# Performance work log

Hardware: AMD Instinct MI355X
Metric: run time of the kernel (lower is better)

Reference implementation:

```python
import jax, jax.numpy as jnp
import numpy as np

J, L = 4, 8
M = N = 128
B = 2
EPS = 1e-6  # abs_eps smoothing: |z|_eps = sqrt(re^2 + im^2 + eps)


def indices_third_order(J, L):
    # For each bandpass filter i = j1*L + l1, pair with every filter of scale
    # j2 >= j1 (all L angles) plus the lowpass (index J*L).
    # Count = J*L*(L*(J+1)/2 + 1) == num_coefficients.
    i_list, j_list = [], []
    for j1 in range(J):
        for l1 in range(L):
            i = j1 * L + l1
            for j2 in range(j1, J):
                for l2 in range(L):
                    i_list.append(i)
                    j_list.append(j2 * L + l2)
            i_list.append(i)
            j_list.append(J * L)
    return np.asarray(i_list), np.asarray(j_list)


def make_filters(J, L, M, N):
    # Real frequency-domain Morlet-like Gaussian bumps at J scales x L angles,
    # plus one lowpass. Shape (1, J*L+1, M, N), float32.
    kx = 2.0 * np.pi * np.fft.fftfreq(M)[:, None]
    ky = 2.0 * np.pi * np.fft.fftfreq(N)[None, :]
    filts = []
    for j in range(J):
        k0 = 0.8 * np.pi / 2.0 ** j
        sigma = 0.5 * k0
        for l in range(L):
            theta = np.pi * l / L
            cx, cy = k0 * np.cos(theta), k0 * np.sin(theta)
            filts.append(np.exp(-((kx - cx) ** 2 + (ky - cy) ** 2) / (2.0 * sigma ** 2)))
    sigma_lp = 0.8 * np.pi / 2.0 ** J
    filts.append(np.exp(-(kx ** 2 + ky ** 2) / (2.0 * sigma_lp ** 2)))
    return np.stack(filts)[None].astype(np.float32)


def abs_eps(z):
    return jnp.sqrt(z.real ** 2 + z.imag ** 2 + EPS)


def setup_inputs() -> dict:
    key = jax.random.key(0)
    x = jax.random.normal(key, (B, 1, M, N), dtype=jnp.float32)
    filters = jnp.asarray(make_filters(J, L, M, N))  # (1, 33, M, N)
    return {"x": x, "filters": filters}


def reference(x, filters):
    idx0, idx1 = indices_third_order(J, L)
    # first-order filtering: (B, nf, M, N) complex
    xf = jnp.fft.ifft2(filters * jnp.fft.fft2(x))
    xa = abs_eps(xf)  # real (B, nf, M, N)
    # cross-scale correlation: (B, nf_i, nf_j, M, N)
    inner = jnp.fft.ifft2(filters[:, None] * jnp.fft.fft2(xa)[:, :, None])
    out = jnp.real(jnp.conj(xf)[:, None] * inner).mean(axis=(-2, -1))  # (B, nf, nf)
    return out[:, idx0, idx1]  # (B, 672)
```

## Files before the change

kernel.cpp:

```cpp
#include <hip/hip_runtime.h>
#include <math.h>


#define PI_F 3.14159265358979323846f

__device__ __forceinline__ void make_tw(int lane, float* twr, float* twi) {
#pragma unroll
  for (int s = 0; s < 6; ++s) {
    int h = 32 >> s;
    float ang = -PI_F * (float)(lane & (h - 1)) / (float)h;
    float sv, cv;
    sincosf(ang, &sv, &cv);
    twr[s] = cv; twi[s] = sv;
  }
  float ang = -PI_F * (float)lane / 64.0f;
  float sv, cv;
  sincosf(ang, &sv, &cv);
  twr[6] = cv; twi[6] = sv;
}

template <int S>
__device__ __forceinline__ void fft128_dif(float& ar, float& ai, float& br, float& bi,
                                           const float* twr, const float* twi, int lane) {
  float s6r = twr[6], s6i = (S > 0) ? twi[6] : -twi[6];
  float ur = ar + br, ui = ai + bi;
  float vr = ar - br, vi = ai - bi;
  ar = ur; ai = ui;
  br = vr * s6r - vi * s6i;
  bi = vr * s6i + vi * s6r;
#pragma unroll
  for (int s = 0; s < 6; ++s) {
    int h = 32 >> s;
    float wr = twr[s], wi = (S > 0) ? twi[s] : -twi[s];
    bool hi = (lane & h) != 0;
    float pr, pi2;
    pr = __shfl_xor(ar, h, 64); pi2 = __shfl_xor(ai, h, 64);
    if (!hi) { ar += pr; ai += pi2; }
    else { float dr = pr - ar, di = pi2 - ai; ar = dr * wr - di * wi; ai = dr * wi + di * wr; }
    pr = __shfl_xor(br, h, 64); pi2 = __shfl_xor(bi, h, 64);
    if (!hi) { br += pr; bi += pi2; }
    else { float dr = pr - br, di = pi2 - bi; br = dr * wr - di * wi; bi = dr * wi + di * wr; }
  }
}

__device__ __forceinline__ void transpose_r2c(float (&dr)[16], float (&di)[16],
    float (&er)[8], float (&ei)[8], float (&fr)[8], float (&fi2)[8],
    float2 (*tile)[128], int lane, int w) {
#pragma unroll
  for (int ch = 0; ch < 2; ++ch) {
    if ((w >> 3) == ch) {
#pragma unroll
      for (int t = 0; t < 8; ++t) {
        int r = w * 8 + t;
        int rr = r & 63, sw = r & 15;
        tile[rr][lane ^ sw] = make_float2(dr[2 * t], di[2 * t]);
        tile[rr][(lane + 64) ^ sw] = make_float2(dr[2 * t + 1], di[2 * t + 1]);
      }
    }
    __syncthreads();
    {
      int sw = lane & 15;
#pragma unroll
      for (int ci = 0; ci < 8; ++ci) {
        int c = w * 8 + ci;
        float2 v = tile[lane][c ^ sw];
        if (ch == 0) { er[ci] = v.x; ei[ci] = v.y; }
        else { fr[ci] = v.x; fi2[ci] = v.y; }
      }
    }
    __syncthreads();
  }
}

__global__ __launch_bounds__(1024, 2) void k_prep(const float* __restrict__ x,
    float2* __restrict__ X, float* __restrict__ out) {
  __shared__ float2 tile[64][128];
  int tid = threadIdx.x;
  if (blockIdx.x == 2) {
    if (tid < 1344) out[tid] = 0.f;
    if (tid < 320) out[tid + 1024] = 0.f;
    return;
  }
  int b = blockIdx.x;
  int lane = tid & 63, w = tid >> 6;
  float twr[7], twi[7]; make_tw(lane, twr, twi);
  const float* xb = x + b * 16384;
  float dr[16], di[16];
  float er[8], ei[8], fr[8], fi2[8];
#pragma unroll
  for (int t = 0; t < 8; ++t) {
    int r = w * 8 + t;
    float ar = xb[r * 128 + lane], ai2 = 0.f, br = xb[r * 128 + lane + 64], bi = 0.f;
    fft128_dif<1>(ar, ai2, br, bi, twr, twi, lane);
    dr[2 * t] = ar; di[2 * t] = ai2; dr[2 * t + 1] = br; di[2 * t + 1] = bi;
  }
  transpose_r2c(dr, di, er, ei, fr, fi2, tile, lane, w);
  int u0 = __brev((unsigned)lane) >> 25;
#pragma unroll
  for (int ci = 0; ci < 8; ++ci) {
    int c = w * 8 + ci;
    float ar = er[ci], ai2 = ei[ci], br = fr[ci], bi = fi2[ci];
    fft128_dif<1>(ar, ai2, br, bi, twr, twi, lane);
    int vn = __brev((unsigned)c) >> 25;
    X[b * 16384 + u0 * 128 + vn] = make_float2(ar, ai2);
    X[b * 16384 + (u0 + 1) * 128 + vn] = make_float2(br, bi);
  }
}

__global__ __launch_bounds__(1024, 2) void k_fields(const float2* __restrict__ X,
    const float* __restrict__ F, float* __restrict__ dfld, float* __restrict__ xa) {
  __shared__ float2 tile[64][128];
  int tid = threadIdx.x, lane = tid & 63, w = tid >> 6;
  bool isd = (blockIdx.x < 66);
  int b, f;
  float* optr;
  if (isd) {
    b = blockIdx.x / 33; f = blockIdx.x - b * 33;
    optr = dfld + blockIdx.x * 16384;
  } else {
    int q = blockIdx.x - 66; b = q >> 5; f = q & 31;
    optr = xa + q * 16384;
  }
  const float* Fb = F + f * 16384;
  float twr[7], twi[7]; make_tw(lane, twr, twi);
  const float2* Xb = X + b * 16384;
  float dr[16], di[16];
  float er[8], ei[8], fr[8], fi2[8];

#pragma unroll
  for (int t = 0; t < 8; ++t) {
    int r = w * 8 + t;
    float2 x0 = Xb[r * 128 + lane];
    float2 x1 = Xb[r * 128 + lane + 64];
    float f0 = Fb[r * 128 + lane], f1 = Fb[r * 128 + lane + 64];
    if (isd) { f0 *= f0; f1 *= f1; }
    float ar = x0.x * f0, ai2 = x0.y * f0, br = x1.x * f1, bi = x1.y * f1;
    fft128_dif<-1>(ar, ai2, br, bi, twr, twi, lane);
    dr[2 * t] = ar; di[2 * t] = ai2; dr[2 * t + 1] = br; di[2 * t + 1] = bi;
  }
  transpose_r2c(dr, di, er, ei, fr, fi2, tile, lane, w);

  const float sc = 1.0f / 16384.0f;
#pragma unroll
  for (int ci = 0; ci < 8; ++ci) {
    int c = w * 8 + ci;
    float ar = er[ci], ai2 = ei[ci], br = fr[ci], bi = fi2[ci];
    fft128_dif<-1>(ar, ai2, br, bi, twr, twi, lane);
    if (isd) {
      optr[c * 128 + lane] = ar;
      optr[c * 128 + lane + 64] = br;
    } else {
      float t0r = ar * sc, t0i = ai2 * sc, t1r = br * sc, t1i = bi * sc;
      optr[c * 128 + lane] = sqrtf(t0r * t0r + t0i * t0i + 1e-6f);
      optr[c * 128 + lane + 64] = sqrtf(t1r * t1r + t1i * t1i + 1e-6f);
    }
  }
}

__global__ __launch_bounds__(512) void k_dot(const float* __restrict__ xa,
    const float* __restrict__ dfld, float* __restrict__ out) {
  int im = blockIdx.x >> 2;
  int slice = blockIdx.x & 3;
  int b = im >> 5, i = im & 31;
  int t = threadIdx.x;
  const float* xr = xa + im * 16384 + slice * 4096;
  const float* db = dfld + b * 33 * 16384 + slice * 4096;
  float acc[33];
#pragma unroll
  for (int j = 0; j < 33; ++j) acc[j] = 0.f;
#pragma unroll
  for (int it = 0; it < 8; ++it) {
    int k = it * 512 + t;
    float xv = xr[k];
#pragma unroll
    for (int j = 0; j < 33; ++j) acc[j] += xv * db[j * 16384 + k];
  }
#pragma unroll
  for (int j = 0; j < 33; ++j) {
#pragma unroll
    for (int off = 32; off > 0; off >>= 1) acc[j] += __shfl_xor(acc[j], off, 64);
  }
  __shared__ float red[8][33];
  int w = t >> 6, lane = t & 63;
  if (lane == 0) {
#pragma unroll
    for (int j = 0; j < 33; ++j) red[w][j] = acc[j];
  }
  __syncthreads();
  if (t < 33) {
    float s = 0.f;
#pragma unroll
    for (int w2 = 0; w2 < 8; ++w2) s += red[w2][t];
    int j = t;
    int j1 = i >> 3, l1 = i & 7;
    const int pref[4] = {0, 264, 464, 600};
    int per = (4 - j1) * 8 + 1;
    int start = pref[j1] + l1 * per;
    int pos = -1;
    if (j == 32) pos = start + per - 1;
    else {
      int j2 = j >> 3;
      if (j2 >= j1) pos = start + (j2 - j1) * 8 + (j & 7);
    }
    if (pos >= 0)
      atomicAdd(out + b * 672 + pos, s * (1.0f / 16384.0f) * (1.0f / 16384.0f));
  }
}

extern "C" void kernel_launch(void* const* d_in, const int* in_sizes, int n_in,
                              void* d_out, int out_size, void* d_ws, size_t ws_size,
                              hipStream_t stream) {
  (void)in_sizes; (void)n_in; (void)out_size; (void)ws_size;
  const float* x = (const float*)d_in[0];
  const float* F = (const float*)d_in[1];
  float* out = (float*)d_out;
  char* ws = (char*)d_ws;
  float2* X = (float2*)(ws + 0);
  float* dfld = (float*)(ws + 262144);
  float* xa = (float*)(ws + 4587520);

  hipLaunchKernelGGL(k_prep, dim3(3), dim3(1024), 0, stream, x, X, out);
  hipLaunchKernelGGL(k_fields, dim3(130), dim3(1024), 0, stream, X, F, dfld, xa);
  hipLaunchKernelGGL(k_dot, dim3(256), dim3(512), 0, stream, xa, dfld, out);
}
```

Measured before the change: 115.8 us.

## Fuse three kernels into one cooperative kernel with grid-wide syncs

Replaces the three-launch pipeline (forward FFT, filtered inverse FFTs, dot reduction) with a single cooperative kernel of 256 blocks of 1024 threads that separates the phases with grid.sync. This removes two kernel launch gaps. The dot phase is restructured to use float4 loads and an LDS atomic reduction, and the twiddle sincos switches to the fast intrinsic. In exchange it needs all 256 large blocks co-resident, pays grid-barrier cost, and may lose some twiddle accuracy.

```diff
diff --git a/kernel.cpp b/kernel.cpp
--- a/kernel.cpp
+++ b/kernel.cpp
@@ -1,5 +1,8 @@
 #include <hip/hip_runtime.h>
+#include <hip/hip_cooperative_groups.h>
 #include <math.h>
+
+namespace cg = cooperative_groups;
 
 
 #define PI_F 3.14159265358979323846f
@@ -10,12 +13,12 @@
     int h = 32 >> s;
     float ang = -PI_F * (float)(lane & (h - 1)) / (float)h;
     float sv, cv;
-    sincosf(ang, &sv, &cv);
+    __sincosf(ang, &sv, &cv);
     twr[s] = cv; twi[s] = sv;
   }
   float ang = -PI_F * (float)lane / 64.0f;
   float sv, cv;
-  sincosf(ang, &sv, &cv);
+  __sincosf(ang, &sv, &cv);
   twr[6] = cv; twi[6] = sv;
 }
 
@@ -72,138 +75,150 @@
   }
 }
 
-__global__ __launch_bounds__(1024, 2) void k_prep(const float* __restrict__ x,
-    float2* __restrict__ X, float* __restrict__ out) {
+__global__ __launch_bounds__(1024) void k_all(const float* __restrict__ x,
+    const float* __restrict__ F, float2* __restrict__ X, float* __restrict__ dfld,
+    float* __restrict__ xa, float* __restrict__ out) {
+  cg::grid_group grid = cg::this_grid();
   __shared__ float2 tile[64][128];
-  int tid = threadIdx.x;
-  if (blockIdx.x == 2) {
+  int tid = threadIdx.x, lane = tid & 63, w = tid >> 6;
+  int blk = blockIdx.x;
+  float twr[7], twi[7]; make_tw(lane, twr, twi);
+  float dr[16], di[16];
+  float er[8], ei[8], fr[8], fi2[8];
+
+  if (blk < 2) {
+    int b = blk;
+    const float* xb = x + b * 16384;
+#pragma unroll
+    for (int t = 0; t < 8; ++t) {
+      int r = w * 8 + t;
+      float ar = xb[r * 128 + lane], ai2 = 0.f, br = xb[r * 128 + lane + 64], bi = 0.f;
+      fft128_dif<1>(ar, ai2, br, bi, twr, twi, lane);
+      dr[2 * t] = ar; di[2 * t] = ai2; dr[2 * t + 1] = br; di[2 * t + 1] = bi;
+    }
+    transpose_r2c(dr, di, er, ei, fr, fi2, tile, lane, w);
+    int u0 = __brev((unsigned)lane) >> 25;
+#pragma unroll
+    for (int ci = 0; ci < 8; ++ci) {
+      int c = w * 8 + ci;
+      float ar = er[ci], ai2 = ei[ci], br = fr[ci], bi = fi2[ci];
+      fft128_dif<1>(ar, ai2, br, bi, twr, twi, lane);
+      int vn = __brev((unsigned)c) >> 25;
+      X[b * 16384 + u0 * 128 + vn] = make_float2(ar, ai2);
+      X[b * 16384 + (u0 + 1) * 128 + vn] = make_float2(br, bi);
+    }
+  } else if (blk == 2) {
     if (tid < 1344) out[tid] = 0.f;
     if (tid < 320) out[tid + 1024] = 0.f;
-    return;
-  }
-  int b = blockIdx.x;
-  int lane = tid & 63, w = tid >> 6;
-  float twr[7], twi[7]; make_tw(lane, twr, twi);
-  const float* xb = x + b * 16384;
-  float dr[16], di[16];
-  float er[8], ei[8], fr[8], fi2[8];
-#pragma unroll
-  for (int t = 0; t < 8; ++t) {
-    int r = w * 8 + t;
-    float ar = xb[r * 128 + lane], ai2 = 0.f, br = xb[r * 128 + lane + 64], bi = 0.f;
-    fft128_dif<1>(ar, ai2, br, bi, twr, twi, lane);
-    dr[2 * t] = ar; di[2 * t] = ai2; dr[2 * t + 1] = br; di[2 * t + 1] = bi;
-  }
-  transpose_r2c(dr, di, er, ei, fr, fi2, tile, lane, w);
-  int u0 = __brev((unsigned)lane) >> 25;
-#pragma unroll
-  for (int ci = 0; ci < 8; ++ci) {
-    int c = w * 8 + ci;
-    float ar = er[ci], ai2 = ei[ci], br = fr[ci], bi = fi2[ci];
-    fft128_dif<1>(ar, ai2, br, bi, twr, twi, lane);
-    int vn = __brev((unsigned)c) >> 25;
-    X[b * 16384 + u0 * 128 + vn] = make_float2(ar, ai2);
-    X[b * 16384 + (u0 + 1) * 128 + vn] = make_float2(br, bi);
-  }
-}
-
-__global__ __launch_bounds__(1024, 2) void k_fields(const float2* __restrict__ X,
-    const float* __restrict__ F, float* __restrict__ dfld, float* __restrict__ xa) {
-  __shared__ float2 tile[64][128];
-  int tid = threadIdx.x, lane = tid & 63, w = tid >> 6;
-  bool isd = (blockIdx.x < 66);
-  int b, f;
-  float* optr;
-  if (isd) {
-    b = blockIdx.x / 33; f = blockIdx.x - b * 33;
-    optr = dfld + blockIdx.x * 16384;
-  } else {
-    int q = blockIdx.x - 66; b = q >> 5; f = q & 31;
-    optr = xa + q * 16384;
-  }
-  const float* Fb = F + f * 16384;
-  float twr[7], twi[7]; make_tw(lane, twr, twi);
-  const float2* Xb = X + b * 16384;
-  float dr[16], di[16];
-  float er[8], ei[8], fr[8], fi2[8];
-
-#pragma unroll
-  for (int t = 0; t < 8; ++t) {
-    int r = w * 8 + t;
-    float2 x0 = Xb[r * 128 + lane];
-    float2 x1 = Xb[r * 128 + lane + 64];
-    float f0 = Fb[r * 128 + lane], f1 = Fb[r * 128 + lane + 64];
-    if (isd) { f0 *= f0; f1 *= f1; }
-    float ar = x0.x * f0, ai2 = x0.y * f0, br = x1.x * f1, bi = x1.y * f1;
-    fft128_dif<-1>(ar, ai2, br, bi, twr, twi, lane);
-    dr[2 * t] = ar; di[2 * t] = ai2; dr[2 * t + 1] = br; di[2 * t + 1] = bi;
-  }
-  transpose_r2c(dr, di, er, ei, fr, fi2, tile, lane, w);
-
-  const float sc = 1.0f / 16384.0f;
-#pragma unroll
-  for (int ci = 0; ci < 8; ++ci) {
-    int c = w * 8 + ci;
-    float ar = er[ci], ai2 = ei[ci], br = fr[ci], bi = fi2[ci];
-    fft128_dif<-1>(ar, ai2, br, bi, twr, twi, lane);
+  }
+  __threadfence();
+  grid.sync();
+
+  if (blk < 130) {
+    bool isd = (blk < 66);
+    int b, f;
+    float* optr;
     if (isd) {
-      optr[c * 128 + lane] = ar;
-      optr[c * 128 + lane + 64] = br;
+      b = blk / 33; f = blk - b * 33;
+      optr = dfld + blk * 16384;
     } else {
-      float t0r = ar * sc, t0i = ai2 * sc, t1r = br * sc, t1i = bi * sc;
-      optr[c * 128 + lane] = sqrtf(t0r * t0r + t0i * t0i + 1e-6f);
-      optr[c * 128 + lane + 64] = sqrtf(t1r * t1r + t1i * t1i + 1e-6f);
-    }
-  }
-}
-
-__global__ __launch_bounds__(512) void k_dot(const float* __restrict__ xa,
-    const float* __restrict__ dfld, float* __restrict__ out) {
-  int im = blockIdx.x >> 2;
-  int slice = blockIdx.x & 3;
-  int b = im >> 5, i = im & 31;
-  int t = threadIdx.x;
-  const float* xr = xa + im * 16384 + slice * 4096;
-  const float* db = dfld + b * 33 * 16384 + slice * 4096;
-  float acc[33];
-#pragma unroll
-  for (int j = 0; j < 33; ++j) acc[j] = 0.f;
-#pragma unroll
-  for (int it = 0; it < 8; ++it) {
-    int k = it * 512 + t;
-    float xv = xr[k];
-#pragma unroll
-    for (int j = 0; j < 33; ++j) acc[j] += xv * db[j * 16384 + k];
-  }
-#pragma unroll
-  for (int j = 0; j < 33; ++j) {
-#pragma unroll
-    for (int off = 32; off > 0; off >>= 1) acc[j] += __shfl_xor(acc[j], off, 64);
-  }
-  __shared__ float red[8][33];
-  int w = t >> 6, lane = t & 63;
-  if (lane == 0) {
-#pragma unroll
-    for (int j = 0; j < 33; ++j) red[w][j] = acc[j];
-  }
-  __syncthreads();
-  if (t < 33) {
-    float s = 0.f;
-#pragma unroll
-    for (int w2 = 0; w2 < 8; ++w2) s += red[w2][t];
-    int j = t;
-    int j1 = i >> 3, l1 = i & 7;
-    const int pref[4] = {0, 264, 464, 600};
-    int per = (4 - j1) * 8 + 1;
-    int start = pref[j1] + l1 * per;
-    int pos = -1;
-    if (j == 32) pos = start + per - 1;
-    else {
-      int j2 = j >> 3;
-      if (j2 >= j1) pos = start + (j2 - j1) * 8 + (j & 7);
-    }
-    if (pos >= 0)
-      atomicAdd(out + b * 672 + pos, s * (1.0f / 16384.0f) * (1.0f / 16384.0f));
+      int q = blk - 66; b = q >> 5; f = q & 31;
+      optr = xa + q * 16384;
+    }
+    const float* Fb = F + f * 16384;
+    const float2* Xb = X + b * 16384;
+#pragma unroll
+    for (int t = 0; t < 8; ++t) {
+      int r = w * 8 + t;
+      float2 x0 = Xb[r * 128 + lane];
+      float2 x1 = Xb[r * 128 + lane + 64];
+      float f0 = Fb[r * 128 + lane], f1 = Fb[r * 128 + lane + 64];
+      if (isd) { f0 *= f0; f1 *= f1; }
+      float ar = x0.x * f0, ai2 = x0.y * f0, br = x1.x * f1, bi = x1.y * f1;
+      fft128_dif<-1>(ar, ai2, br, bi, twr, twi, lane);
+      dr[2 * t] = ar; di[2 * t] = ai2; dr[2 * t + 1] = br; di[2 * t + 1] = bi;
+    }
+    transpose_r2c(dr, di, er, ei, fr, fi2, tile, lane, w);
+    const float sc = 1.0f / 16384.0f;
+#pragma unroll
+    for (int ci = 0; ci < 8; ++ci) {
+      int c = w * 8 + ci;
+      float ar = er[ci], ai2 = ei[ci], br = fr[ci], bi = fi2[ci];
+      fft128_dif<-1>(ar, ai2, br, bi, twr, twi, lane);
+      if (isd) {
+        optr[c * 128 + lane] = ar;
+        optr[c * 128 + lane + 64] = br;
+      } else {
+        float t0r = ar * sc, t0i = ai2 * sc, t1r = br * sc, t1i = bi * sc;
+        optr[c * 128 + lane] = sqrtf(t0r * t0r + t0i * t0i + 1e-6f);
+        optr[c * 128 + lane + 64] = sqrtf(t1r * t1r + t1i * t1i + 1e-6f);
+      }
+    }
+  }
+  __threadfence();
+  grid.sync();
+
+  {
+    int q = blk & 3;
+    int im = blk >> 2;
+    int b = im >> 5, i = im & 31;
+    int k0 = q * 4096;
+    float* xs = (float*)tile;
+    float* red = xs + 4096;
+    const float4* xr4 = (const float4*)(xa + im * 16384 + k0);
+    const float* db = dfld + b * 33 * 16384 + k0;
+    ((float4*)xs)[tid] = xr4[tid];
+    if (tid < 33) red[tid] = 0.f;
+    __syncthreads();
+    float4 xv = ((const float4*)xs)[tid];
+    {
+      float acc[16];
+#pragma unroll
+      for (int j = 0; j < 16; ++j) acc[j] = 0.f;
+#pragma unroll
+      for (int j = 0; j < 16; ++j) {
+        float4 d4 = ((const float4*)(db + j * 16384))[tid];
+        acc[j] += xv.x * d4.x + xv.y * d4.y + xv.z * d4.z + xv.w * d4.w;
+      }
+#pragma unroll
+      for (int j = 0; j < 16; ++j) {
+#pragma unroll
+        for (int off = 32; off > 0; off >>= 1) acc[j] += __shfl_xor(acc[j], off, 64);
+        if (lane == 0) atomicAdd(&red[j], acc[j]);
+      }
+    }
+    {
+      float acc[17];
+#pragma unroll
+      for (int j = 0; j < 17; ++j) acc[j] = 0.f;
+#pragma unroll
+      for (int j = 0; j < 17; ++j) {
+        float4 d4 = ((const float4*)(db + (16 + j) * 16384))[tid];
+        acc[j] += xv.x * d4.x + xv.y * d4.y + xv.z * d4.z + xv.w * d4.w;
+      }
+#pragma unroll
+      for (int j = 0; j < 17; ++j) {
+#pragma unroll
+        for (int off = 32; off > 0; off >>= 1) acc[j] += __shfl_xor(acc[j], off, 64);
+        if (lane == 0) atomicAdd(&red[16 + j], acc[j]);
+      }
+    }
+    __syncthreads();
+    if (tid < 33) {
+      int j = tid;
+      int j1 = i >> 3, l1 = i & 7;
+      const int pref[4] = {0, 264, 464, 600};
+      int per = (4 - j1) * 8 + 1;
+      int start = pref[j1] + l1 * per;
+      int pos = -1;
+      if (j == 32) pos = start + per - 1;
+      else {
+        int j2 = j >> 3;
+        if (j2 >= j1) pos = start + (j2 - j1) * 8 + (j & 7);
+      }
+      if (pos >= 0)
+        atomicAdd(out + b * 672 + pos, red[j] * (1.0f / 16384.0f) * (1.0f / 16384.0f));
+    }
   }
 }
 
@@ -219,7 +234,6 @@
   float* dfld = (float*)(ws + 262144);
   float* xa = (float*)(ws + 4587520);
 
-  hipLaunchKernelGGL(k_prep, dim3(3), dim3(1024), 0, stream, x, X, out);
-  hipLaunchKernelGGL(k_fields, dim3(130), dim3(1024), 0, stream, X, F, dfld, xa);
-  hipLaunchKernelGGL(k_dot, dim3(256), dim3(512), 0, stream, xa, dfld, out);
-}
+  void* args[] = {(void*)&x, (void*)&F, (void*)&X, (void*)&dfld, (void*)&xa, (void*)&out};
+  hipLaunchCooperativeKernel((const void*)k_all, dim3(256), dim3(1024), args, 0, stream);
+}
```

Result: slower. 325.1 us (+180.8%).

## Vectorize k_dot loads with float4, stage xa in LDS, use fast sincos

Applied to the files above, without the earlier changes.

The k_dot reduction now loads xa and dfld as float4 and stages each block's xa slice in shared memory. Block indexing is reordered so neighbouring blocks share the same b and slice of dfld, and per-wave partial sums are combined with LDS atomics instead of a per-wave table. Twiddle generation switches to the fast __sincosf intrinsic. This cuts global load instruction count and may improve cache locality on dfld, at the cost of slightly less accurate twiddles and a different accumulation order.

```diff
diff --git a/kernel.cpp b/kernel.cpp
--- a/kernel.cpp
+++ b/kernel.cpp
@@ -10,12 +10,12 @@
     int h = 32 >> s;
     float ang = -PI_F * (float)(lane & (h - 1)) / (float)h;
     float sv, cv;
-    sincosf(ang, &sv, &cv);
+    __sincosf(ang, &sv, &cv);
     twr[s] = cv; twi[s] = sv;
   }
   float ang = -PI_F * (float)lane / 64.0f;
   float sv, cv;
-  sincosf(ang, &sv, &cv);
+  __sincosf(ang, &sv, &cv);
   twr[6] = cv; twi[6] = sv;
 }
 
@@ -159,39 +159,37 @@
 
 __global__ __launch_bounds__(512) void k_dot(const float* __restrict__ xa,
     const float* __restrict__ dfld, float* __restrict__ out) {
-  int im = blockIdx.x >> 2;
-  int slice = blockIdx.x & 3;
-  int b = im >> 5, i = im & 31;
-  int t = threadIdx.x;
-  const float* xr = xa + im * 16384 + slice * 4096;
-  const float* db = dfld + b * 33 * 16384 + slice * 4096;
+  __shared__ float4 xs[1024];
+  __shared__ float red[33];
+  int tid = threadIdx.x, lane = tid & 63;
+  int g = blockIdx.x & 7, i = blockIdx.x >> 3;
+  int b = g & 1, q = g >> 1;
+  int im = b * 32 + i, k0 = q * 4096;
+  const float4* xr4 = (const float4*)(xa + im * 16384 + k0);
+  xs[tid] = xr4[tid];
+  xs[tid + 512] = xr4[tid + 512];
+  if (tid < 33) red[tid] = 0.f;
+  __syncthreads();
+  float4 x0 = xs[tid], x1 = xs[tid + 512];
+  const float* db = dfld + b * 33 * 16384 + k0;
   float acc[33];
 #pragma unroll
-  for (int j = 0; j < 33; ++j) acc[j] = 0.f;
-#pragma unroll
-  for (int it = 0; it < 8; ++it) {
-    int k = it * 512 + t;
-    float xv = xr[k];
-#pragma unroll
-    for (int j = 0; j < 33; ++j) acc[j] += xv * db[j * 16384 + k];
-  }
-#pragma unroll
   for (int j = 0; j < 33; ++j) {
-#pragma unroll
-    for (int off = 32; off > 0; off >>= 1) acc[j] += __shfl_xor(acc[j], off, 64);
-  }
-  __shared__ float red[8][33];
-  int w = t >> 6, lane = t & 63;
-  if (lane == 0) {
-#pragma unroll
-    for (int j = 0; j < 33; ++j) red[w][j] = acc[j];
+    const float4* dj = (const float4*)(db + j * 16384);
+    float4 d0 = dj[tid], d1 = dj[tid + 512];
+    acc[j] = x0.x * d0.x + x0.y * d0.y + x0.z * d0.z + x0.w * d0.w
+           + x1.x * d1.x + x1.y * d1.y + x1.z * d1.z + x1.w * d1.w;
+  }
+#pragma unroll
+  for (int j = 0; j < 33; ++j) {
+    float s = acc[j];
+#pragma unroll
+    for (int off = 32; off > 0; off >>= 1) s += __shfl_xor(s, off, 64);
+    if (lane == 0) atomicAdd(&red[j], s);
   }
   __syncthreads();
-  if (t < 33) {
-    float s = 0.f;
-#pragma unroll
-    for (int w2 = 0; w2 < 8; ++w2) s += red[w2][t];
-    int j = t;
+  if (tid < 33) {
+    int j = tid;
     int j1 = i >> 3, l1 = i & 7;
     const int pref[4] = {0, 264, 464, 600};
     int per = (4 - j1) * 8 + 1;
@@ -203,7 +201,7 @@
       if (j2 >= j1) pos = start + (j2 - j1) * 8 + (j & 7);
     }
     if (pos >= 0)
-      atomicAdd(out + b * 672 + pos, s * (1.0f / 16384.0f) * (1.0f / 16384.0f));
+      atomicAdd(out + b * 672 + pos, red[j] * (1.0f / 16384.0f) * (1.0f / 16384.0f));
   }
 }
 
```

Result: slower. 124.8 us (+7.8%).
